# Kernel tuning notes

Measured on AMD Instinct MI355X. Metric: run time of the kernel, lower is better.

Reference implementation:

```python
import jax, jax.numpy as jnp
import numpy as np

N_NODES = 100000
N_EDGES = 1600000
N_GRAPHS = 1024
TIME_DIM = 64
HID = 32
HEADS = 4
NEG_SLOPE = 0.2


def _gat_layer(x, src, dst, W, a_src, a_dst, bias, heads, out_dim):
    # PyG GATConv: h = x @ W, per-head attention, segment softmax over incoming edges at dst.
    N = x.shape[0]
    h = (x @ W).reshape(N, heads, out_dim)                     # [N, H, D]
    alpha_src = jnp.sum(h * a_src, axis=-1)                    # [N, H]
    alpha_dst = jnp.sum(h * a_dst, axis=-1)                    # [N, H]
    e = alpha_src[src] + alpha_dst[dst]                        # [E, H]
    e = jnp.where(e > 0, e, NEG_SLOPE * e)                     # LeakyReLU(0.2)
    m = jax.ops.segment_max(e, dst, num_segments=N)            # [N, H]
    m = jnp.where(jnp.isfinite(m), m, 0.0)
    ex = jnp.exp(e - m[dst])                                   # [E, H]
    s = jax.ops.segment_sum(ex, dst, num_segments=N)           # [N, H]
    alpha = ex / (s[dst] + 1e-16)                              # [E, H]
    msg = h[src] * alpha[..., None]                            # [E, H, D]
    out = jax.ops.segment_sum(msg, dst, num_segments=N)        # [N, H, D]
    return out.reshape(N, heads * out_dim) + bias


def setup_inputs() -> dict:
    key = jax.random.key(0)
    ks = jax.random.split(key, 12)
    x = jax.random.normal(ks[0], (N_NODES, TIME_DIM), jnp.float32)
    edge_index = jax.random.randint(ks[1], (2, N_EDGES), 0, N_NODES, jnp.int32)
    batch = jnp.sort(jax.random.randint(ks[2], (N_NODES,), 0, N_GRAPHS, jnp.int32))
    s = 0.1
    params = {
        "W1": jax.random.normal(ks[3], (TIME_DIM, HEADS * HID), jnp.float32) * s,
        "a_src1": jax.random.normal(ks[4], (HEADS, HID), jnp.float32) * s,
        "a_dst1": jax.random.normal(ks[5], (HEADS, HID), jnp.float32) * s,
        "b1": jnp.zeros((HEADS * HID,), jnp.float32),
        "W2": jax.random.normal(ks[6], (HEADS * HID, HID), jnp.float32) * s,
        "a_src2": jax.random.normal(ks[7], (1, HID), jnp.float32) * s,
        "a_dst2": jax.random.normal(ks[8], (1, HID), jnp.float32) * s,
        "b2": jnp.zeros((HID,), jnp.float32),
        "Wc": jax.random.normal(ks[9], (HID, 1), jnp.float32) * s,
        "bc": jnp.zeros((1,), jnp.float32),
    }
    return dict(x=x, edge_index=edge_index, batch=batch, **params)


def reference(x, edge_index, batch, W1, a_src1, a_dst1, b1, W2, a_src2, a_dst2, b2, Wc, bc):
    N = x.shape[0]
    # PyG GATConv adds self-loops by default.
    loops = jnp.arange(N, dtype=edge_index.dtype)
    src = jnp.concatenate([edge_index[0], loops])
    dst = jnp.concatenate([edge_index[1], loops])

    h1 = jax.nn.relu(_gat_layer(x, src, dst, W1, a_src1, a_dst1, b1, HEADS, HID))
    h2 = jax.nn.relu(_gat_layer(h1, src, dst, W2, a_src2, a_dst2, b2, 1, HID))

    # global_mean_pool over batch ids
    sums = jax.ops.segment_sum(h2, batch, num_segments=N_GRAPHS)          # [G, HID]
    cnts = jax.ops.segment_sum(jnp.ones((N,), h2.dtype), batch, num_segments=N_GRAPHS)
    pooled = sums / jnp.maximum(cnts, 1.0)[:, None]

    return jax.nn.sigmoid(pooled @ Wc + bc)                               # [G, 1]
```

## Files before the change

### kernel.cpp

```cpp
#include <hip/hip_runtime.h>
#include <hip/hip_bf16.h>

#define BSH 7
#define MAXNB 800
#define STILE 8192
#define BCAP 4096

__device__ inline float bf_lo(unsigned u) { return __uint_as_float(u << 16); }
__device__ inline float bf_hi(unsigned u) { return __uint_as_float(u & 0xffff0000u); }


__global__ __launch_bounds__(256) void k_bscatter(const int* __restrict__ ei, int E, int NB,
                                                  int* __restrict__ bcur, int* __restrict__ pairs) {
    __shared__ int lh[MAXNB];
    __shared__ int lbase[MAXNB];
    int t = threadIdx.x;
    int e0 = blockIdx.x * STILE;
    int e1 = min(E, e0 + STILE);
    for (int i = t; i < NB; i += 256) lh[i] = 0;
    __syncthreads();
    for (int e = e0 + t; e < e1; e += 256) atomicAdd(&lh[ei[E + e] >> BSH], 1);
    __syncthreads();
    for (int i = t; i < NB; i += 256) {
        int c = lh[i];
        lbase[i] = c ? atomicAdd(&bcur[i], c) : 0;
    }
    __syncthreads();
    for (int i = t; i < NB; i += 256) lh[i] = 0;
    __syncthreads();
    for (int e = e0 + t; e < e1; e += 256) {
        int s = ei[e], d = ei[E + e];
        int bk = d >> BSH;
        int off = atomicAdd(&lh[bk], 1);
        pairs[(size_t)bk * BCAP + lbase[bk] + off] = (s << BSH) | (d & ((1 << BSH) - 1));
    }
}

__global__ __launch_bounds__(256) void k_build(const int* __restrict__ pairs,
                                               const int* __restrict__ bcur, int N, int NB,
                                               int2* __restrict__ span, int* __restrict__ csr) {
    __shared__ int lcnt[128];
    __shared__ int loff[128];
    __shared__ int lcur[128];
    int b = blockIdx.x, t = threadIdx.x;
    int node0 = b << BSH;
    size_t base = (size_t)b * BCAP;
    int ne = bcur[b];
    if (t < 128) lcnt[t] = 0;
    __syncthreads();
    for (int i = t; i < ne; i += 256) atomicAdd(&lcnt[pairs[base + i] & 127], 1);
    __syncthreads();
    if (t < 128) loff[t] = lcnt[t];
    __syncthreads();
#pragma unroll
    for (int off = 1; off < 128; off <<= 1) {
        int v = (t < 128 && t >= off) ? loff[t - off] : 0;
        __syncthreads();
        if (t < 128) loff[t] += v;
        __syncthreads();
    }
    if (t < 128) {
        int excl = loff[t] - lcnt[t];
        int n = node0 + t;
        if (n < N) span[n] = make_int2((int)base + excl, (int)base + excl + lcnt[t]);
        lcur[t] = excl;
    }
    __syncthreads();
    for (int i = t; i < ne; i += 256) {
        int p = pairs[base + i];
        int pos = (int)base + atomicAdd(&lcur[p & 127], 1);
        csr[pos] = ((unsigned)p) >> BSH;
    }
}


__global__ __launch_bounds__(256) void k_gemm1(const float* __restrict__ x, const float* __restrict__ W1,
                                               const float* __restrict__ asw, const float* __restrict__ adw,
                                               unsigned short* __restrict__ h8, float2* __restrict__ aP,
                                               float2* __restrict__ aDp, int N) {
    __shared__ float xt[64][20];
    int t = threadIdx.x;
    int n0 = blockIdx.x * 16;
    for (int i = t; i < 16 * 64; i += 256) {
        int r = i >> 6, k = i & 63;
        xt[k][r] = (n0 + r < N) ? x[(size_t)(n0 + r) * 64 + k] : 0.f;
    }
    __syncthreads();
    int col = t & 127, half = t >> 7;
    int head = col >> 5, d = col & 31;
    const float* Wc = W1 + col;
    float acc[8] = {0, 0, 0, 0, 0, 0, 0, 0};
#pragma unroll 4
    for (int k = 0; k < 64; k++) {
        float w = Wc[k * 128];
        float4 xa = *(const float4*)&xt[k][half * 8];
        float4 xb = *(const float4*)&xt[k][half * 8 + 4];
        acc[0] = fmaf(xa.x, w, acc[0]); acc[1] = fmaf(xa.y, w, acc[1]);
        acc[2] = fmaf(xa.z, w, acc[2]); acc[3] = fmaf(xa.w, w, acc[3]);
        acc[4] = fmaf(xb.x, w, acc[4]); acc[5] = fmaf(xb.y, w, acc[5]);
        acc[6] = fmaf(xb.z, w, acc[6]); acc[7] = fmaf(xb.w, w, acc[7]);
    }
#pragma unroll
    for (int i = 0; i < 8; i++) {
        int n = n0 + half * 8 + i;
        float other = __shfl_xor(acc[i], 1);
        if (((col & 1) == 0) && n < N) {
            int pk = __builtin_amdgcn_cvt_pk_fp8_f32(acc[i], other, 0, false);
            h8[(size_t)n * 64 + (col >> 1)] = (unsigned short)pk;
        }
    }
    float aw = asw[col], dw = adw[col];
#pragma unroll
    for (int i = 0; i < 8; i++) {
        float as = acc[i] * aw, ad = acc[i] * dw;
#pragma unroll
        for (int mm = 16; mm >= 1; mm >>= 1) { as += __shfl_xor(as, mm); ad += __shfl_xor(ad, mm); }
        int n = n0 + half * 8 + i;
        if (d == 0 && n < N) {
            aP[n * 4 + head]  = make_float2(__expf(as), __expf(0.2f * as));
            aDp[n * 4 + head] = make_float2(__expf(ad), __expf(0.2f * ad));
        }
    }
}


__global__ __launch_bounds__(256) void k_gat1(const unsigned* __restrict__ h8,
                                              const float2* __restrict__ aP, const float2* __restrict__ aDp,
                                              const int2* __restrict__ span, const int* __restrict__ csr,
                                              const float* __restrict__ b1, uint2* __restrict__ out, int N) {
    int t = threadIdx.x;
    int n = blockIdx.x * 4 + (t >> 6);
    if (n >= N) return;
    int lane = t & 63;
    int e2 = lane >> 5, c = lane & 31;
    int head = c >> 3;
    float2 dnp = aDp[n * 4 + head];
    float ec = dnp.x, ed = dnp.y;
    float2 psf = aP[n * 4 + head];
    float w_self = fmaxf(psf.x * ec, psf.y * ed);
    int2 sp = span[n];
    int beg = sp.x, end = sp.y;

    float a0 = 0.f, a1 = 0.f, a2 = 0.f, a3 = 0.f, s = 0.f;
    if (e2 == 0) {
        unsigned u = h8[(size_t)n * 32 + c];
        auto f01 = __builtin_amdgcn_cvt_pk_f32_fp8((int)u, false);
        auto f23 = __builtin_amdgcn_cvt_pk_f32_fp8((int)u, true);
        a0 = w_self * f01[0]; a1 = w_self * f01[1];
        a2 = w_self * f23[0]; a3 = w_self * f23[1];
        s = w_self;
    }
    int j = beg + e2;
    for (; j + 6 < end; j += 8) {
        int s0 = csr[j], s1 = csr[j + 2], s2 = csr[j + 4], s3 = csr[j + 6];
        float2 p0 = aP[s0 * 4 + head];
        float2 p1 = aP[s1 * 4 + head];
        float2 p2 = aP[s2 * 4 + head];
        float2 p3 = aP[s3 * 4 + head];
        unsigned u0 = h8[(size_t)s0 * 32 + c];
        unsigned u1 = h8[(size_t)s1 * 32 + c];
        unsigned u2 = h8[(size_t)s2 * 32 + c];
        unsigned u3 = h8[(size_t)s3 * 32 + c];
        float w0 = fmaxf(p0.x * ec, p0.y * ed);
        float w1 = fmaxf(p1.x * ec, p1.y * ed);
        float w2 = fmaxf(p2.x * ec, p2.y * ed);
        float w3 = fmaxf(p3.x * ec, p3.y * ed);
        s += w0 + w1 + w2 + w3;
        {
            auto f01 = __builtin_amdgcn_cvt_pk_f32_fp8((int)u0, false);
            auto f23 = __builtin_amdgcn_cvt_pk_f32_fp8((int)u0, true);
            a0 = fmaf(w0, f01[0], a0); a1 = fmaf(w0, f01[1], a1);
            a2 = fmaf(w0, f23[0], a2); a3 = fmaf(w0, f23[1], a3);
        }
        {
            auto f01 = __builtin_amdgcn_cvt_pk_f32_fp8((int)u1, false);
            auto f23 = __builtin_amdgcn_cvt_pk_f32_fp8((int)u1, true);
            a0 = fmaf(w1, f01[0], a0); a1 = fmaf(w1, f01[1], a1);
            a2 = fmaf(w1, f23[0], a2); a3 = fmaf(w1, f23[1], a3);
        }
        {
            auto f01 = __builtin_amdgcn_cvt_pk_f32_fp8((int)u2, false);
            auto f23 = __builtin_amdgcn_cvt_pk_f32_fp8((int)u2, true);
            a0 = fmaf(w2, f01[0], a0); a1 = fmaf(w2, f01[1], a1);
            a2 = fmaf(w2, f23[0], a2); a3 = fmaf(w2, f23[1], a3);
        }
        {
            auto f01 = __builtin_amdgcn_cvt_pk_f32_fp8((int)u3, false);
            auto f23 = __builtin_amdgcn_cvt_pk_f32_fp8((int)u3, true);
            a0 = fmaf(w3, f01[0], a0); a1 = fmaf(w3, f01[1], a1);
            a2 = fmaf(w3, f23[0], a2); a3 = fmaf(w3, f23[1], a3);
        }
    }
    for (; j < end; j += 2) {
        int sj = csr[j];
        float2 p = aP[sj * 4 + head];
        unsigned u = h8[(size_t)sj * 32 + c];
        float w = fmaxf(p.x * ec, p.y * ed);
        s += w;
        auto f01 = __builtin_amdgcn_cvt_pk_f32_fp8((int)u, false);
        auto f23 = __builtin_amdgcn_cvt_pk_f32_fp8((int)u, true);
        a0 = fmaf(w, f01[0], a0); a1 = fmaf(w, f01[1], a1);
        a2 = fmaf(w, f23[0], a2); a3 = fmaf(w, f23[1], a3);
    }
    a0 += __shfl_xor(a0, 32); a1 += __shfl_xor(a1, 32);
    a2 += __shfl_xor(a2, 32); a3 += __shfl_xor(a3, 32);
    s  += __shfl_xor(s, 32);
    if (e2 == 0) {
        float inv = 1.f / (s + 1e-16f);
        float4 b = ((const float4*)b1)[c];
        float o0 = fmaxf(fmaf(a0, inv, b.x), 0.f);
        float o1 = fmaxf(fmaf(a1, inv, b.y), 0.f);
        float o2 = fmaxf(fmaf(a2, inv, b.z), 0.f);
        float o3 = fmaxf(fmaf(a3, inv, b.w), 0.f);
        unsigned lo0 = (unsigned)__bfloat16_as_ushort(__float2bfloat16(o0));
        unsigned hi0 = ((unsigned)__bfloat16_as_ushort(__float2bfloat16(o1))) << 16;
        unsigned lo1 = (unsigned)__bfloat16_as_ushort(__float2bfloat16(o2));
        unsigned hi1 = ((unsigned)__bfloat16_as_ushort(__float2bfloat16(o3))) << 16;
        out[(size_t)n * 32 + c] = make_uint2(lo0 | hi0, lo1 | hi1);
    }
}


__global__ __launch_bounds__(256) void k_gemm2(const unsigned* __restrict__ h1b, const float* __restrict__ W2,
                                               const float* __restrict__ asw, const float* __restrict__ adw,
                                               unsigned short* __restrict__ h8, float2* __restrict__ aP,
                                               float2* __restrict__ aDp, int N) {
    __shared__ float xt[128][36];
    int t = threadIdx.x;
    int n0 = blockIdx.x * 32;
    for (int i = t; i < 32 * 64; i += 256) {
        int r = i >> 6, c = i & 63;
        unsigned u = (n0 + r < N) ? h1b[(size_t)(n0 + r) * 64 + c] : 0u;
        xt[2 * c][r]     = bf_lo(u);
        xt[2 * c + 1][r] = bf_hi(u);
    }
    __syncthreads();
    int col = t & 31, grp = t >> 5;
    const float* Wc = W2 + col;
    float acc[4] = {0, 0, 0, 0};
#pragma unroll 4
    for (int k = 0; k < 128; k++) {
        float w = Wc[k * 32];
        float4 xv = *(const float4*)&xt[k][grp * 4];
        acc[0] = fmaf(xv.x, w, acc[0]); acc[1] = fmaf(xv.y, w, acc[1]);
        acc[2] = fmaf(xv.z, w, acc[2]); acc[3] = fmaf(xv.w, w, acc[3]);
    }
    float aw = asw[col], dw = adw[col];
#pragma unroll
    for (int i = 0; i < 4; i++) {
        int n = n0 + grp * 4 + i;
        float other = __shfl_xor(acc[i], 1);
        if (((col & 1) == 0) && n < N) {
            int pk = __builtin_amdgcn_cvt_pk_fp8_f32(acc[i], other, 0, false);
            h8[(size_t)n * 16 + (col >> 1)] = (unsigned short)pk;
        }
        float as = acc[i] * aw, ad = acc[i] * dw;
#pragma unroll
        for (int mm = 16; mm >= 1; mm >>= 1) { as += __shfl_xor(as, mm); ad += __shfl_xor(ad, mm); }
        if (col == 0 && n < N) {
            aP[n]  = make_float2(__expf(as), __expf(0.2f * as));
            aDp[n] = make_float2(__expf(ad), __expf(0.2f * ad));
        }
    }
}


__global__ __launch_bounds__(256) void k_gat2(const unsigned* __restrict__ h8,
                                              const float2* __restrict__ aP, const float2* __restrict__ aDp,
                                              const int2* __restrict__ span, const int* __restrict__ csr,
                                              const float* __restrict__ b2, float* __restrict__ out, int N) {
    int t = threadIdx.x;
    int n = blockIdx.x * 4 + (t >> 6);
    if (n >= N) return;
    int lane = t & 63;
    int e8 = lane >> 3, c = lane & 7;
    float2 dnp = aDp[n];
    float ec = dnp.x, ed = dnp.y;
    float2 psf = aP[n];
    float w_self = fmaxf(psf.x * ec, psf.y * ed);
    int2 sp = span[n];
    int beg = sp.x, end = sp.y;

    float a0 = 0.f, a1 = 0.f, a2 = 0.f, a3 = 0.f, s = 0.f;
    if (e8 == 0) {
        unsigned u = h8[(size_t)n * 8 + c];
        auto f01 = __builtin_amdgcn_cvt_pk_f32_fp8((int)u, false);
        auto f23 = __builtin_amdgcn_cvt_pk_f32_fp8((int)u, true);
        a0 = w_self * f01[0]; a1 = w_self * f01[1];
        a2 = w_self * f23[0]; a3 = w_self * f23[1];
        s = w_self;
    }
    int j = beg + e8;
    for (; j + 8 < end; j += 16) {
        int s0 = csr[j], s1 = csr[j + 8];
        float2 p0 = aP[s0], p1 = aP[s1];
        unsigned u0 = h8[(size_t)s0 * 8 + c];
        unsigned u1 = h8[(size_t)s1 * 8 + c];
        float w0 = fmaxf(p0.x * ec, p0.y * ed);
        float w1 = fmaxf(p1.x * ec, p1.y * ed);
        s += w0 + w1;
        {
            auto f01 = __builtin_amdgcn_cvt_pk_f32_fp8((int)u0, false);
            auto f23 = __builtin_amdgcn_cvt_pk_f32_fp8((int)u0, true);
            a0 = fmaf(w0, f01[0], a0); a1 = fmaf(w0, f01[1], a1);
            a2 = fmaf(w0, f23[0], a2); a3 = fmaf(w0, f23[1], a3);
        }
        {
            auto f01 = __builtin_amdgcn_cvt_pk_f32_fp8((int)u1, false);
            auto f23 = __builtin_amdgcn_cvt_pk_f32_fp8((int)u1, true);
            a0 = fmaf(w1, f01[0], a0); a1 = fmaf(w1, f01[1], a1);
            a2 = fmaf(w1, f23[0], a2); a3 = fmaf(w1, f23[1], a3);
        }
    }
    for (; j < end; j += 8) {
        int sj = csr[j];
        float2 p = aP[sj];
        unsigned u = h8[(size_t)sj * 8 + c];
        float w = fmaxf(p.x * ec, p.y * ed);
        s += w;
        auto f01 = __builtin_amdgcn_cvt_pk_f32_fp8((int)u, false);
        auto f23 = __builtin_amdgcn_cvt_pk_f32_fp8((int)u, true);
        a0 = fmaf(w, f01[0], a0); a1 = fmaf(w, f01[1], a1);
        a2 = fmaf(w, f23[0], a2); a3 = fmaf(w, f23[1], a3);
    }
#pragma unroll
    for (int off = 8; off < 64; off <<= 1) {
        a0 += __shfl_xor(a0, off); a1 += __shfl_xor(a1, off);
        a2 += __shfl_xor(a2, off); a3 += __shfl_xor(a3, off);
        s  += __shfl_xor(s, off);
    }
    if (e8 == 0) {
        float inv = 1.f / (s + 1e-16f);
        float4 b = ((const float4*)b2)[c];
        float4 o;
        o.x = fmaxf(fmaf(a0, inv, b.x), 0.f);
        o.y = fmaxf(fmaf(a1, inv, b.y), 0.f);
        o.z = fmaxf(fmaf(a2, inv, b.z), 0.f);
        o.w = fmaxf(fmaf(a3, inv, b.w), 0.f);
        ((float4*)out)[(size_t)n * 8 + c] = o;
    }
}


__global__ void k_pool(const float* __restrict__ h2r, const int* __restrict__ batch, int N,
                       const float* __restrict__ Wc, const float* __restrict__ bc,
                       float* __restrict__ out) {
    int g = blockIdx.x;
    int t = threadIdx.x, d = t & 31, r = t >> 5;
    int lo = 0, hi = N;
    while (lo < hi) { int mid = (lo + hi) >> 1; if (batch[mid] < g) lo = mid + 1; else hi = mid; }
    int start = lo;
    hi = N;
    while (lo < hi) { int mid = (lo + hi) >> 1; if (batch[mid] < g + 1) lo = mid + 1; else hi = mid; }
    int end = lo;
    float sum = 0.f;
    for (int i = start + r; i < end; i += 2) sum += h2r[(size_t)i * 32 + d];
    sum += __shfl_xor(sum, 32);
    float cnt = (float)(end - start);
    float mean = sum / fmaxf(cnt, 1.f);
    float v = mean * Wc[d];
#pragma unroll
    for (int m = 16; m >= 1; m >>= 1) v += __shfl_xor(v, m);
    if (t == 0) out[g] = 1.f / (1.f + expf(-(v + bc[0])));
}


extern "C" void kernel_launch(void* const* d_in, const int* in_sizes, int n_in,
                              void* d_out, int out_size, void* d_ws, size_t ws_size,
                              hipStream_t stream) {
    const float* x    = (const float*)d_in[0];
    const int*   ei   = (const int*)d_in[1];
    const int*   batch= (const int*)d_in[2];
    const float* W1   = (const float*)d_in[3];
    const float* as1  = (const float*)d_in[4];
    const float* ad1  = (const float*)d_in[5];
    const float* b1   = (const float*)d_in[6];
    const float* W2   = (const float*)d_in[7];
    const float* as2  = (const float*)d_in[8];
    const float* ad2  = (const float*)d_in[9];
    const float* b2   = (const float*)d_in[10];
    const float* Wc   = (const float*)d_in[11];
    const float* bc   = (const float*)d_in[12];

    const int N = in_sizes[0] / 64;
    const int E = in_sizes[1] / 2;
    const int G = out_size;
    const int NB = (N + 127) >> BSH;

    size_t off = 0;
    char* base = (char*)d_ws;
    auto alloc = [&](size_t bytes) -> char* {
        char* p = base + off;
        off += (bytes + 255) & ~(size_t)255;
        return p;
    };
    int*      bcur  = (int*)alloc((size_t)NB * 4);
    int*      pairs = (int*)alloc((size_t)NB * BCAP * 4);
    int2*     span  = (int2*)alloc((size_t)N * 8);
    int*      csr   = (int*)alloc((size_t)NB * BCAP * 4);
    unsigned short* h8_1 = (unsigned short*)alloc((size_t)N * 128);
    unsigned* h1b   = (unsigned*)alloc((size_t)N * 64 * 4);
    float2*   aP1   = (float2*)alloc((size_t)N * 4 * 8);
    float2*   aDp1  = (float2*)alloc((size_t)N * 4 * 8);
    unsigned short* h8_2 = (unsigned short*)alloc((size_t)N * 32);
    float*    h2r   = (float*)alloc((size_t)N * 32 * 4);
    float2*   aP2   = (float2*)alloc((size_t)N * 8);
    float2*   aDp2  = (float2*)alloc((size_t)N * 8);
    (void)ws_size; (void)n_in;

    hipMemsetAsync(bcur, 0, (size_t)NB * 4, stream);
    k_bscatter<<<(E + STILE - 1) / STILE, 256, 0, stream>>>(ei, E, NB, bcur, pairs);
    k_build<<<NB, 256, 0, stream>>>(pairs, bcur, N, NB, span, csr);

    k_gemm1<<<(N + 15) / 16, 256, 0, stream>>>(x, W1, as1, ad1, h8_1, aP1, aDp1, N);
    k_gat1<<<(N + 3) / 4, 256, 0, stream>>>((const unsigned*)h8_1, aP1, aDp1, span, csr, b1, (uint2*)h1b, N);

    k_gemm2<<<(N + 31) / 32, 256, 0, stream>>>(h1b, W2, as2, ad2, h8_2, aP2, aDp2, N);
    k_gat2<<<(N + 3) / 4, 256, 0, stream>>>((const unsigned*)h8_2, aP2, aDp2, span, csr, b2, h2r, N);

    k_pool<<<G, 64, 0, stream>>>(h2r, batch, N, Wc, bc, (float*)d_out);
}
```

Before: 263.1 us.

## Split layer-1 GAT aggregation per head with head-major fp8 feature layout

The layer-1 projection now stores fp8 features head-major ([head][N][32]), and the aggregation kernel gets a second grid dimension over heads. Each wavefront handles one head of one node, with 8 lanes per edge and 8 edges in flight. The aim is a smaller per-head gather footprint (32 bytes per source row per head) that fits cache better, plus more parallelism from the quadrupled grid. In exchange, the CSR indices and attention scalars are re-read once per head, and the cross-lane reduction across 8 edge groups is deeper.

```diff
diff --git a/kernel.cpp b/kernel.cpp
--- a/kernel.cpp
+++ b/kernel.cpp
@@ -104,9 +104,9 @@
     for (int i = 0; i < 8; i++) {
         int n = n0 + half * 8 + i;
         float other = __shfl_xor(acc[i], 1);
-        if (((col & 1) == 0) && n < N) {
+        if (((d & 1) == 0) && n < N) {
             int pk = __builtin_amdgcn_cvt_pk_fp8_f32(acc[i], other, 0, false);
-            h8[(size_t)n * 64 + (col >> 1)] = (unsigned short)pk;
+            h8[((size_t)head * N + n) * 16 + (d >> 1)] = (unsigned short)pk;
         }
     }
     float aw = asw[col], dw = adw[col];
@@ -131,41 +131,35 @@
     int t = threadIdx.x;
     int n = blockIdx.x * 4 + (t >> 6);
     if (n >= N) return;
+    int h = blockIdx.y;
     int lane = t & 63;
-    int e2 = lane >> 5, c = lane & 31;
-    int head = c >> 3;
-    float2 dnp = aDp[n * 4 + head];
+    int e8 = lane >> 3, c = lane & 7;
+    float2 dnp = aDp[n * 4 + h];
     float ec = dnp.x, ed = dnp.y;
-    float2 psf = aP[n * 4 + head];
+    float2 psf = aP[n * 4 + h];
     float w_self = fmaxf(psf.x * ec, psf.y * ed);
     int2 sp = span[n];
     int beg = sp.x, end = sp.y;
 
+    const unsigned* hh = h8 + (size_t)h * N * 8;
     float a0 = 0.f, a1 = 0.f, a2 = 0.f, a3 = 0.f, s = 0.f;
-    if (e2 == 0) {
-        unsigned u = h8[(size_t)n * 32 + c];
+    if (e8 == 0) {
+        unsigned u = hh[(size_t)n * 8 + c];
         auto f01 = __builtin_amdgcn_cvt_pk_f32_fp8((int)u, false);
         auto f23 = __builtin_amdgcn_cvt_pk_f32_fp8((int)u, true);
         a0 = w_self * f01[0]; a1 = w_self * f01[1];
         a2 = w_self * f23[0]; a3 = w_self * f23[1];
         s = w_self;
     }
-    int j = beg + e2;
-    for (; j + 6 < end; j += 8) {
-        int s0 = csr[j], s1 = csr[j + 2], s2 = csr[j + 4], s3 = csr[j + 6];
-        float2 p0 = aP[s0 * 4 + head];
-        float2 p1 = aP[s1 * 4 + head];
-        float2 p2 = aP[s2 * 4 + head];
-        float2 p3 = aP[s3 * 4 + head];
-        unsigned u0 = h8[(size_t)s0 * 32 + c];
-        unsigned u1 = h8[(size_t)s1 * 32 + c];
-        unsigned u2 = h8[(size_t)s2 * 32 + c];
-        unsigned u3 = h8[(size_t)s3 * 32 + c];
+    int j = beg + e8;
+    for (; j + 8 < end; j += 16) {
+        int s0 = csr[j], s1 = csr[j + 8];
+        float2 p0 = aP[s0 * 4 + h], p1 = aP[s1 * 4 + h];
+        unsigned u0 = hh[(size_t)s0 * 8 + c];
+        unsigned u1 = hh[(size_t)s1 * 8 + c];
         float w0 = fmaxf(p0.x * ec, p0.y * ed);
         float w1 = fmaxf(p1.x * ec, p1.y * ed);
-        float w2 = fmaxf(p2.x * ec, p2.y * ed);
-        float w3 = fmaxf(p3.x * ec, p3.y * ed);
-        s += w0 + w1 + w2 + w3;
+        s += w0 + w1;
         {
             auto f01 = __builtin_amdgcn_cvt_pk_f32_fp8((int)u0, false);
             auto f23 = __builtin_amdgcn_cvt_pk_f32_fp8((int)u0, true);
@@ -178,23 +172,11 @@
             a0 = fmaf(w1, f01[0], a0); a1 = fmaf(w1, f01[1], a1);
             a2 = fmaf(w1, f23[0], a2); a3 = fmaf(w1, f23[1], a3);
         }
-        {
-            auto f01 = __builtin_amdgcn_cvt_pk_f32_fp8((int)u2, false);
-            auto f23 = __builtin_amdgcn_cvt_pk_f32_fp8((int)u2, true);
-            a0 = fmaf(w2, f01[0], a0); a1 = fmaf(w2, f01[1], a1);
-            a2 = fmaf(w2, f23[0], a2); a3 = fmaf(w2, f23[1], a3);
-        }
-        {
-            auto f01 = __builtin_amdgcn_cvt_pk_f32_fp8((int)u3, false);
-            auto f23 = __builtin_amdgcn_cvt_pk_f32_fp8((int)u3, true);
-            a0 = fmaf(w3, f01[0], a0); a1 = fmaf(w3, f01[1], a1);
-            a2 = fmaf(w3, f23[0], a2); a3 = fmaf(w3, f23[1], a3);
-        }
-    }
-    for (; j < end; j += 2) {
+    }
+    for (; j < end; j += 8) {
         int sj = csr[j];
-        float2 p = aP[sj * 4 + head];
-        unsigned u = h8[(size_t)sj * 32 + c];
+        float2 p = aP[sj * 4 + h];
+        unsigned u = hh[(size_t)sj * 8 + c];
         float w = fmaxf(p.x * ec, p.y * ed);
         s += w;
         auto f01 = __builtin_amdgcn_cvt_pk_f32_fp8((int)u, false);
@@ -202,12 +184,15 @@
         a0 = fmaf(w, f01[0], a0); a1 = fmaf(w, f01[1], a1);
         a2 = fmaf(w, f23[0], a2); a3 = fmaf(w, f23[1], a3);
     }
-    a0 += __shfl_xor(a0, 32); a1 += __shfl_xor(a1, 32);
-    a2 += __shfl_xor(a2, 32); a3 += __shfl_xor(a3, 32);
-    s  += __shfl_xor(s, 32);
-    if (e2 == 0) {
+#pragma unroll
+    for (int off = 8; off < 64; off <<= 1) {
+        a0 += __shfl_xor(a0, off); a1 += __shfl_xor(a1, off);
+        a2 += __shfl_xor(a2, off); a3 += __shfl_xor(a3, off);
+        s  += __shfl_xor(s, off);
+    }
+    if (e8 == 0) {
         float inv = 1.f / (s + 1e-16f);
-        float4 b = ((const float4*)b1)[c];
+        float4 b = ((const float4*)b1)[h * 8 + c];
         float o0 = fmaxf(fmaf(a0, inv, b.x), 0.f);
         float o1 = fmaxf(fmaf(a1, inv, b.y), 0.f);
         float o2 = fmaxf(fmaf(a2, inv, b.z), 0.f);
@@ -216,7 +201,7 @@
         unsigned hi0 = ((unsigned)__bfloat16_as_ushort(__float2bfloat16(o1))) << 16;
         unsigned lo1 = (unsigned)__bfloat16_as_ushort(__float2bfloat16(o2));
         unsigned hi1 = ((unsigned)__bfloat16_as_ushort(__float2bfloat16(o3))) << 16;
-        out[(size_t)n * 32 + c] = make_uint2(lo0 | hi0, lo1 | hi1);
+        out[(size_t)n * 32 + h * 8 + c] = make_uint2(lo0 | hi0, lo1 | hi1);
     }
 }
 
@@ -413,7 +398,7 @@
     k_build<<<NB, 256, 0, stream>>>(pairs, bcur, N, NB, span, csr);
 
     k_gemm1<<<(N + 15) / 16, 256, 0, stream>>>(x, W1, as1, ad1, h8_1, aP1, aDp1, N);
-    k_gat1<<<(N + 3) / 4, 256, 0, stream>>>((const unsigned*)h8_1, aP1, aDp1, span, csr, b1, (uint2*)h1b, N);
+    k_gat1<<<dim3((N + 3) / 4, 4), 256, 0, stream>>>((const unsigned*)h8_1, aP1, aDp1, span, csr, b1, (uint2*)h1b, N);
 
     k_gemm2<<<(N + 31) / 32, 256, 0, stream>>>(h1b, W2, as2, ad2, h8_2, aP2, aDp2, N);
     k_gat2<<<(N + 3) / 4, 256, 0, stream>>>((const unsigned*)h8_2, aP2, aDp2, span, csr, b2, h2r, N);
```

After: 354.2 us. 1.35x slower.
